# Kernel tuning notes

Measured on AMD Instinct MI355X. Metric: run time of the kernel, lower is better.

Reference implementation:

```python
import jax, jax.numpy as jnp
import numpy as np

B, A, C = 1, 196416, 90
H = W = 1024
SCORE_THRESHOLD = 0.05
MAX_DETECTIONS = 100
# RetinaNet-style BBoxTransform normalization (mean=0, std=[0.1,0.1,0.2,0.2])
STD = (0.1, 0.1, 0.2, 0.2)


def setup_inputs() -> dict:
    key = jax.random.key(0)
    k1, k2, k3, k4, k5, k6, k7 = jax.random.split(key, 7)
    x = jax.random.normal(k1, (B, 3, H, W), dtype=jnp.float32)
    regression = jax.random.normal(k2, (B, A, 4), dtype=jnp.float32) * 0.1
    classification = jax.random.normal(k3, (B, A, C), dtype=jnp.float32)
    # valid anchor boxes (x1, y1, x2, y2)
    cx = jax.random.uniform(k4, (B, A), minval=0.0, maxval=float(W))
    cy = jax.random.uniform(k5, (B, A), minval=0.0, maxval=float(H))
    aw = jax.random.uniform(k6, (B, A), minval=16.0, maxval=256.0)
    ah = jax.random.uniform(k7, (B, A), minval=16.0, maxval=256.0)
    anchors = jnp.stack([cx - 0.5 * aw, cy - 0.5 * ah, cx + 0.5 * aw, cy + 0.5 * ah], axis=2).astype(jnp.float32)
    return {"x": x, "regression": regression, "classification": classification, "anchors": anchors}


def _decode_clip(anchors, regression, img_h, img_w):
    # BBoxTransform: deltas (dx, dy, dw, dh) scaled by std, applied to anchor center/size
    wa = anchors[..., 2] - anchors[..., 0]
    ha = anchors[..., 3] - anchors[..., 1]
    cxa = anchors[..., 0] + 0.5 * wa
    cya = anchors[..., 1] + 0.5 * ha
    dx = regression[..., 0] * STD[0]
    dy = regression[..., 1] * STD[1]
    dw = regression[..., 2] * STD[2]
    dh = regression[..., 3] * STD[3]
    cx = cxa + dx * wa
    cy = cya + dy * ha
    w = jnp.exp(dw) * wa
    h = jnp.exp(dh) * ha
    # ClipBoxes: x1,y1 clamped at 0; x2,y2 clamped at image width/height
    x1 = jnp.maximum(cx - 0.5 * w, 0.0)
    y1 = jnp.maximum(cy - 0.5 * h, 0.0)
    x2 = jnp.minimum(cx + 0.5 * w, float(img_w))
    y2 = jnp.minimum(cy + 0.5 * h, float(img_h))
    return jnp.stack([x1, y1, x2, y2], axis=2)  # [B, A, 4]


def reference(x, regression, classification, anchors):
    img_h, img_w = x.shape[2], x.shape[3]
    boxes = _decode_clip(anchors, regression, img_h, img_w)  # [1, A, 4]
    probs = jax.nn.sigmoid(classification)                    # [1, A, C]
    scores = jnp.max(probs, axis=2)                           # [1, A]
    classes = jnp.argmax(probs, axis=2)                       # [1, A]
    valid_scores = jnp.where(scores > SCORE_THRESHOLD, scores, 0.0)
    vb = boxes[0]            # [A, 4]
    vc = classes[0]          # [A]
    vs = valid_scores[0]     # [A]
    k = min(MAX_DETECTIONS, vs.shape[0])
    _, top_idx = jax.lax.top_k(vs, k)
    final_boxes = vb[top_idx]
    final_scores = vs[top_idx]
    final_classes = vc[top_idx]
    return (final_boxes, final_scores, final_classes)
```

## Files before the change

kernel.cpp:

```cpp
#include <hip/hip_runtime.h>
#include <cmath>

#define A_CNT 196416
#define C_CNT 90
#define PAIRS (A_CNT / 2)
#define WITERS 12276
#define TOPK 100u
#define CAPB 2048

#define OFF_HIST1 785664u
#define OFF_CTRL  789760u
#define OFF_CANDA 789824u
#define OFF_CANDB 790336u

__global__ __launch_bounds__(256, 4) void k_reduce(const float* __restrict__ cls,
                                                   unsigned* __restrict__ keys,
                                                   unsigned* __restrict__ hist1) {
    __shared__ unsigned lhist[576];
    const int t = threadIdx.x;
    for (int j = t; j < 576; j += 256) lhist[j] = 0u;
    __syncthreads();

    const int lane = t & 63;
    const int g = lane >> 3, s = lane & 7;
    const int wid = blockIdx.x * 4 + (t >> 6);
    const int nw = gridDim.x * 4;
    const float4* __restrict__ cls4 = (const float4*)cls;

    for (int w = wid; w < WITERS; w += nw) {
        const int p = w * 8 + g;
        const float4* __restrict__ r4 = cls4 + (size_t)p * 45;
        float m0 = -INFINITY, m1 = -INFINITY;
#pragma unroll
        for (int i = 0; i < 6; ++i) {
            const int j = s + 8 * i;
            if (j < 45) {
                float4 v = r4[j];
                float a01 = fmaxf(v.x, v.y), a23 = fmaxf(v.z, v.w);
                float all = fmaxf(a01, a23);
                if (j < 22)      m0 = fmaxf(m0, all);
                else if (j > 22) m1 = fmaxf(m1, all);
                else { m0 = fmaxf(m0, a01); m1 = fmaxf(m1, a23); }
            }
        }
#pragma unroll
        for (int d = 1; d < 8; d <<= 1) {
            m0 = fmaxf(m0, __shfl_xor(m0, d));
            m1 = fmaxf(m1, __shfl_xor(m1, d));
        }
        if (s == 0) {
            float p0 = 1.0f / (1.0f + expf(-m0));
            float p1 = 1.0f / (1.0f + expf(-m1));
            unsigned k0 = (p0 > 0.05f) ? __float_as_uint(p0) : 0u;
            unsigned k1 = (p1 > 0.05f) ? __float_as_uint(p1) : 0u;
            *(uint2*)(keys + 2 * p) = make_uint2(k0, k1);
            unsigned h0 = k0 ? (min(k0 >> 16, 0x3F80u) - 0x3D4Bu) : 0u;
            unsigned h1 = k1 ? (min(k1 >> 16, 0x3F80u) - 0x3D4Bu) : 0u;
            atomicAdd(&lhist[h0], 1u);
            atomicAdd(&lhist[h1], 1u);
        }
    }
    __syncthreads();
    for (int j = t; j < 576; j += 256) {
        unsigned c = lhist[j];
        if (c) atomicAdd(&hist1[j], c);
    }
}

__global__ __launch_bounds__(256) void k_scan(const unsigned* __restrict__ hist,
                                              unsigned* __restrict__ ctrl) {
    __shared__ unsigned sdata[256];
    __shared__ unsigned sbin[2];
    const int t = threadIdx.x;
    const unsigned target = TOPK;

    uint4 u = ((const uint4*)hist)[t];
    unsigned s = u.x + u.y + u.z + u.w;
    sdata[t] = s;
    for (int d = 1; d < 256; d <<= 1) {
        __syncthreads();
        unsigned add = (t + d < 256) ? sdata[t + d] : 0u;
        __syncthreads();
        sdata[t] += add;
    }
    __syncthreads();
    {
        unsigned mysuf  = sdata[t];
        unsigned nxtsuf = (t < 255) ? sdata[t + 1] : 0u;
        if (nxtsuf < target && mysuf >= target) { sbin[0] = (unsigned)t; sbin[1] = nxtsuf; }
    }
    __syncthreads();
    const unsigned chunkB = sbin[0];
    const unsigned gAbove = sbin[1];

    unsigned v = (t < 4) ? hist[chunkB * 4 + t] : 0u;
    sdata[t] = v;
    for (int d = 1; d < 256; d <<= 1) {
        __syncthreads();
        unsigned add = (t + d < 256) ? sdata[t + d] : 0u;
        __syncthreads();
        sdata[t] += add;
    }
    __syncthreads();
    {
        unsigned mysuf  = sdata[t] + gAbove;
        unsigned nxtsuf = ((t < 255) ? sdata[t + 1] : 0u) + gAbove;
        if (nxtsuf < target && mysuf >= target) {
            unsigned bin = chunkB * 4 + (unsigned)t;
            ctrl[0] = bin ? (bin + 0x3D4Bu) : 0u;
            ctrl[1] = nxtsuf;
        }
    }
}

__global__ __launch_bounds__(256) void k_gather(const unsigned* __restrict__ keys,
                                                unsigned* __restrict__ ctrl,
                                                unsigned* __restrict__ candA,
                                                unsigned* __restrict__ candB) {
    const unsigned binB = ctrl[0];
    const int i4 = blockIdx.x * 256 + threadIdx.x;
    if (i4 >= A_CNT / 4) return;
    uint4 k = ((const uint4*)keys)[i4];
    const unsigned base = (unsigned)(4 * i4);
#pragma unroll
    for (int j = 0; j < 4; ++j) {
        unsigned kk = (j == 0) ? k.x : (j == 1) ? k.y : (j == 2) ? k.z : k.w;
        unsigned t16 = kk >> 16;
        if (t16 > binB) {
            unsigned q = atomicAdd(&ctrl[5], 1u);
            if (q < 128u) candA[q] = base + j;
        } else if (t16 == binB) {
            unsigned q = atomicAdd(&ctrl[6], 1u);
            if (q < (unsigned)CAPB) candB[q] = base + j;
        }
    }
}

__global__ __launch_bounds__(256) void k_final(const float* __restrict__ cls,
                                               const float* __restrict__ reg,
                                               const float* __restrict__ anc,
                                               const unsigned* __restrict__ ctrl,
                                               const unsigned* __restrict__ candA,
                                               const unsigned* __restrict__ candB,
                                               const unsigned* __restrict__ keys,
                                               float* __restrict__ out) {
    __shared__ unsigned sAi[128], sAk[128];
    __shared__ unsigned sBi[CAPB], sBk[CAPB];
    __shared__ unsigned sel[TOPK];
    const int t = threadIdx.x;
    const unsigned nA = min(ctrl[5], 128u);
    const unsigned nB = min(ctrl[6], (unsigned)CAPB);
    const unsigned need = TOPK - nA;

    if (t < (int)nA) { unsigned i = candA[t]; sAi[t] = i; sAk[t] = keys[i]; }
    for (unsigned e = (unsigned)t; e < nB; e += 256u) {
        unsigned i = candB[e]; sBi[e] = i; sBk[e] = keys[i];
    }
    __syncthreads();

    if (t < (int)nA) {
        unsigned mi = sAi[t], mk = sAk[t], r = 0;
        for (unsigned j = 0; j < nA; ++j) {
            unsigned ok = sAk[j];
            if (ok > mk || (ok == mk && sAi[j] < mi)) r++;
        }
        sel[r] = mi;
    }
    for (unsigned e = (unsigned)t; e < nB; e += 256u) {
        unsigned mi = sBi[e], mk = sBk[e], r = 0;
        for (unsigned j = 0; j < nB; ++j) {
            unsigned ok = sBk[j];
            if (ok > mk || (ok == mk && sBi[j] < mi)) r++;
        }
        if (r < need) sel[nA + r] = mi;
    }
    __syncthreads();

    if (t < (int)TOPK) {
        const unsigned a = sel[t];
        const float2* row = (const float2*)(cls + (size_t)a * C_CNT);
        float bv = -INFINITY; int bi = 0;
#pragma unroll 5
        for (int c = 0; c < 45; ++c) {
            float2 v = row[c];
            if (v.x > bv) { bv = v.x; bi = 2 * c; }
            if (v.y > bv) { bv = v.y; bi = 2 * c + 1; }
        }
        float score = __uint_as_float(keys[a]);
        float x1a = anc[a * 4 + 0], y1a = anc[a * 4 + 1];
        float x2a = anc[a * 4 + 2], y2a = anc[a * 4 + 3];
        float wa = x2a - x1a, ha = y2a - y1a;
        float cxa = x1a + 0.5f * wa, cya = y1a + 0.5f * ha;
        float dx = reg[a * 4 + 0] * 0.1f, dy = reg[a * 4 + 1] * 0.1f;
        float dw = reg[a * 4 + 2] * 0.2f, dh = reg[a * 4 + 3] * 0.2f;
        float cx = cxa + dx * wa, cy = cya + dy * ha;
        float w = expf(dw) * wa, h = expf(dh) * ha;
        out[t * 4 + 0] = fmaxf(cx - 0.5f * w, 0.0f);
        out[t * 4 + 1] = fmaxf(cy - 0.5f * h, 0.0f);
        out[t * 4 + 2] = fminf(cx + 0.5f * w, 1024.0f);
        out[t * 4 + 3] = fminf(cy + 0.5f * h, 1024.0f);
        out[400 + t] = score;
        out[500 + t] = (float)bi;
    }
}

extern "C" void kernel_launch(void* const* d_in, const int* in_sizes, int n_in,
                              void* d_out, int out_size, void* d_ws, size_t ws_size,
                              hipStream_t stream) {
    const float* reg = (const float*)d_in[1];
    const float* cls = (const float*)d_in[2];
    const float* anc = (const float*)d_in[3];
    float* out = (float*)d_out;
    char* ws = (char*)d_ws;
    unsigned* keys  = (unsigned*)ws;
    unsigned* hist1 = (unsigned*)(ws + OFF_HIST1);
    unsigned* ctrl  = (unsigned*)(ws + OFF_CTRL);
    unsigned* candA = (unsigned*)(ws + OFF_CANDA);
    unsigned* candB = (unsigned*)(ws + OFF_CANDB);

    hipMemsetAsync(hist1, 0, 4096 + 64, stream);
    k_reduce<<<2048, 256, 0, stream>>>(cls, keys, hist1);
    k_scan<<<1, 256, 0, stream>>>(hist1, ctrl);
    k_gather<<<192, 256, 0, stream>>>(keys, ctrl, candA, candB);
    k_final<<<1, 256, 0, stream>>>(cls, reg, anc, ctrl, candA, candB, keys, out);
}
```

Before: 160.3 us.

## Stage classification tiles in LDS with coalesced loads before row-max reduction

```diff
diff --git a/kernel.cpp b/kernel.cpp
--- a/kernel.cpp
+++ b/kernel.cpp
@@ -3,62 +3,50 @@
 
 #define A_CNT 196416
 #define C_CNT 90
-#define PAIRS (A_CNT / 2)
-#define WITERS 12276
 #define TOPK 100u
 #define CAPB 2048
+#define TB 64
+#define NTILE (A_CNT / TB)
 
 #define OFF_HIST1 785664u
 #define OFF_CTRL  789760u
 #define OFF_CANDA 789824u
 #define OFF_CANDB 790336u
 
-__global__ __launch_bounds__(256, 4) void k_reduce(const float* __restrict__ cls,
-                                                   unsigned* __restrict__ keys,
-                                                   unsigned* __restrict__ hist1) {
+__global__ __launch_bounds__(256) void k_reduce(const float* __restrict__ cls,
+                                                unsigned* __restrict__ keys,
+                                                unsigned* __restrict__ hist1) {
+    __shared__ alignas(16) float smem[TB * C_CNT];
     __shared__ unsigned lhist[576];
     const int t = threadIdx.x;
     for (int j = t; j < 576; j += 256) lhist[j] = 0u;
-    __syncthreads();
-
-    const int lane = t & 63;
-    const int g = lane >> 3, s = lane & 7;
-    const int wid = blockIdx.x * 4 + (t >> 6);
-    const int nw = gridDim.x * 4;
-    const float4* __restrict__ cls4 = (const float4*)cls;
-
-    for (int w = wid; w < WITERS; w += nw) {
-        const int p = w * 8 + g;
-        const float4* __restrict__ r4 = cls4 + (size_t)p * 45;
-        float m0 = -INFINITY, m1 = -INFINITY;
+
+    const float4* __restrict__ g4 = (const float4*)cls + (size_t)blockIdx.x * 1440;
+    float4* __restrict__ s4 = (float4*)smem;
 #pragma unroll
-        for (int i = 0; i < 6; ++i) {
-            const int j = s + 8 * i;
-            if (j < 45) {
-                float4 v = r4[j];
-                float a01 = fmaxf(v.x, v.y), a23 = fmaxf(v.z, v.w);
-                float all = fmaxf(a01, a23);
-                if (j < 22)      m0 = fmaxf(m0, all);
-                else if (j > 22) m1 = fmaxf(m1, all);
-                else { m0 = fmaxf(m0, a01); m1 = fmaxf(m1, a23); }
-            }
-        }
-#pragma unroll
-        for (int d = 1; d < 8; d <<= 1) {
-            m0 = fmaxf(m0, __shfl_xor(m0, d));
-            m1 = fmaxf(m1, __shfl_xor(m1, d));
-        }
-        if (s == 0) {
-            float p0 = 1.0f / (1.0f + expf(-m0));
-            float p1 = 1.0f / (1.0f + expf(-m1));
-            unsigned k0 = (p0 > 0.05f) ? __float_as_uint(p0) : 0u;
-            unsigned k1 = (p1 > 0.05f) ? __float_as_uint(p1) : 0u;
-            *(uint2*)(keys + 2 * p) = make_uint2(k0, k1);
-            unsigned h0 = k0 ? (min(k0 >> 16, 0x3F80u) - 0x3D4Bu) : 0u;
-            unsigned h1 = k1 ? (min(k1 >> 16, 0x3F80u) - 0x3D4Bu) : 0u;
-            atomicAdd(&lhist[h0], 1u);
-            atomicAdd(&lhist[h1], 1u);
-        }
+    for (int i = 0; i < 6; ++i) {
+        int c = t + 256 * i;
+        if (c < 1440) s4[c] = g4[c];
+    }
+    __syncthreads();
+
+    const int r = t >> 2, h = t & 3;
+    const float2* row = (const float2*)(smem + r * C_CNT) + h * 12;
+    const int n2 = (h < 3) ? 12 : 9;
+    float m = -INFINITY;
+#pragma unroll 3
+    for (int i = 0; i < n2; ++i) {
+        float2 v = row[i];
+        m = fmaxf(m, fmaxf(v.x, v.y));
+    }
+    m = fmaxf(m, __shfl_xor(m, 1));
+    m = fmaxf(m, __shfl_xor(m, 2));
+    if (h == 0) {
+        float pr = 1.0f / (1.0f + expf(-m));
+        unsigned k = (pr > 0.05f) ? __float_as_uint(pr) : 0u;
+        keys[blockIdx.x * TB + r] = k;
+        unsigned hi = k ? (min(k >> 16, 0x3F80u) - 0x3D4Bu) : 0u;
+        atomicAdd(&lhist[hi], 1u);
     }
     __syncthreads();
     for (int j = t; j < 576; j += 256) {
@@ -219,7 +207,7 @@
     unsigned* candB = (unsigned*)(ws + OFF_CANDB);
 
     hipMemsetAsync(hist1, 0, 4096 + 64, stream);
-    k_reduce<<<2048, 256, 0, stream>>>(cls, keys, hist1);
+    k_reduce<<<NTILE, 256, 0, stream>>>(cls, keys, hist1);
     k_scan<<<1, 256, 0, stream>>>(hist1, ctrl);
     k_gather<<<192, 256, 0, stream>>>(keys, ctrl, candA, candB);
     k_final<<<1, 256, 0, stream>>>(cls, reg, anc, ctrl, candA, candB, keys, out);
```

After: 168.2 us. +4.9%, slower.

## Fuse scan and final stages into preceding kernels via last-block-done counters

Applied to the files above, without the earlier changes.

```diff
diff --git a/kernel.cpp b/kernel.cpp
--- a/kernel.cpp
+++ b/kernel.cpp
@@ -7,16 +7,25 @@
 #define WITERS 12276
 #define TOPK 100u
 #define CAPB 2048
+#define NB_RED 1536
+#define NB_GAT 192
 
 #define OFF_HIST1 785664u
 #define OFF_CTRL  789760u
 #define OFF_CANDA 789824u
 #define OFF_CANDB 790336u
 
+#define AGENT_LD(p)    __hip_atomic_load((p), __ATOMIC_RELAXED, __HIP_MEMORY_SCOPE_AGENT)
+#define AGENT_ST(p, v) __hip_atomic_store((p), (v), __ATOMIC_RELAXED, __HIP_MEMORY_SCOPE_AGENT)
+
 __global__ __launch_bounds__(256, 4) void k_reduce(const float* __restrict__ cls,
                                                    unsigned* __restrict__ keys,
-                                                   unsigned* __restrict__ hist1) {
+                                                   unsigned* __restrict__ hist1,
+                                                   unsigned* __restrict__ ctrl) {
     __shared__ unsigned lhist[576];
+    __shared__ unsigned sdata[256];
+    __shared__ unsigned sbin[2];
+    __shared__ int sflag;
     const int t = threadIdx.x;
     for (int j = t; j < 576; j += 256) lhist[j] = 0u;
     __syncthreads();
@@ -24,7 +33,7 @@
     const int lane = t & 63;
     const int g = lane >> 3, s = lane & 7;
     const int wid = blockIdx.x * 4 + (t >> 6);
-    const int nw = gridDim.x * 4;
+    const int nw = NB_RED * 4;
     const float4* __restrict__ cls4 = (const float4*)cls;
 
     for (int w = wid; w < WITERS; w += nw) {
@@ -65,18 +74,16 @@
         unsigned c = lhist[j];
         if (c) atomicAdd(&hist1[j], c);
     }
-}
-
-__global__ __launch_bounds__(256) void k_scan(const unsigned* __restrict__ hist,
-                                              unsigned* __restrict__ ctrl) {
-    __shared__ unsigned sdata[256];
-    __shared__ unsigned sbin[2];
-    const int t = threadIdx.x;
+    __syncthreads();
+    if (t == 0) sflag = (atomicAdd(&ctrl[8], 1u) == NB_RED - 1u) ? 1 : 0;
+    __syncthreads();
+    if (!sflag) return;
+
     const unsigned target = TOPK;
-
-    uint4 u = ((const uint4*)hist)[t];
-    unsigned s = u.x + u.y + u.z + u.w;
-    sdata[t] = s;
+    unsigned ssum = 0;
+#pragma unroll
+    for (int j = 0; j < 4; ++j) ssum += AGENT_LD(&hist1[t * 4 + j]);
+    sdata[t] = ssum;
     for (int d = 1; d < 256; d <<= 1) {
         __syncthreads();
         unsigned add = (t + d < 256) ? sdata[t + d] : 0u;
@@ -92,8 +99,7 @@
     __syncthreads();
     const unsigned chunkB = sbin[0];
     const unsigned gAbove = sbin[1];
-
-    unsigned v = (t < 4) ? hist[chunkB * 4 + t] : 0u;
+    unsigned v = (t < 4) ? AGENT_LD(&hist1[chunkB * 4 + t]) : 0u;
     sdata[t] = v;
     for (int d = 1; d < 256; d <<= 1) {
         __syncthreads();
@@ -113,48 +119,50 @@
     }
 }
 
-__global__ __launch_bounds__(256) void k_gather(const unsigned* __restrict__ keys,
+__global__ __launch_bounds__(256) void k_gather(const float* __restrict__ cls,
+                                                const float* __restrict__ reg,
+                                                const float* __restrict__ anc,
+                                                const unsigned* __restrict__ keys,
                                                 unsigned* __restrict__ ctrl,
                                                 unsigned* __restrict__ candA,
-                                                unsigned* __restrict__ candB) {
-    const unsigned binB = ctrl[0];
-    const int i4 = blockIdx.x * 256 + threadIdx.x;
-    if (i4 >= A_CNT / 4) return;
-    uint4 k = ((const uint4*)keys)[i4];
-    const unsigned base = (unsigned)(4 * i4);
-#pragma unroll
-    for (int j = 0; j < 4; ++j) {
-        unsigned kk = (j == 0) ? k.x : (j == 1) ? k.y : (j == 2) ? k.z : k.w;
-        unsigned t16 = kk >> 16;
-        if (t16 > binB) {
-            unsigned q = atomicAdd(&ctrl[5], 1u);
-            if (q < 128u) candA[q] = base + j;
-        } else if (t16 == binB) {
-            unsigned q = atomicAdd(&ctrl[6], 1u);
-            if (q < (unsigned)CAPB) candB[q] = base + j;
-        }
-    }
-}
-
-__global__ __launch_bounds__(256) void k_final(const float* __restrict__ cls,
-                                               const float* __restrict__ reg,
-                                               const float* __restrict__ anc,
-                                               const unsigned* __restrict__ ctrl,
-                                               const unsigned* __restrict__ candA,
-                                               const unsigned* __restrict__ candB,
-                                               const unsigned* __restrict__ keys,
-                                               float* __restrict__ out) {
+                                                unsigned* __restrict__ candB,
+                                                float* __restrict__ out) {
     __shared__ unsigned sAi[128], sAk[128];
     __shared__ unsigned sBi[CAPB], sBk[CAPB];
     __shared__ unsigned sel[TOPK];
+    __shared__ int sflag;
     const int t = threadIdx.x;
-    const unsigned nA = min(ctrl[5], 128u);
-    const unsigned nB = min(ctrl[6], (unsigned)CAPB);
+
+    const unsigned binB = ctrl[0];
+    const int i4 = blockIdx.x * 256 + t;
+    if (i4 < A_CNT / 4) {
+        uint4 k = ((const uint4*)keys)[i4];
+        const unsigned base = (unsigned)(4 * i4);
+#pragma unroll
+        for (int j = 0; j < 4; ++j) {
+            unsigned kk = (j == 0) ? k.x : (j == 1) ? k.y : (j == 2) ? k.z : k.w;
+            unsigned t16 = kk >> 16;
+            if (t16 > binB) {
+                unsigned q = atomicAdd(&ctrl[5], 1u);
+                if (q < 128u) AGENT_ST(&candA[q], base + j);
+            } else if (t16 == binB) {
+                unsigned q = atomicAdd(&ctrl[6], 1u);
+                if (q < (unsigned)CAPB) AGENT_ST(&candB[q], base + j);
+            }
+        }
+    }
+    __syncthreads();
+    if (t == 0) sflag = (atomicAdd(&ctrl[9], 1u) == (unsigned)NB_GAT - 1u) ? 1 : 0;
+    __syncthreads();
+    if (!sflag) return;
+
+    const unsigned nA = min(AGENT_LD(&ctrl[5]), 128u);
+    const unsigned nB = min(AGENT_LD(&ctrl[6]), (unsigned)CAPB);
     const unsigned need = TOPK - nA;
 
-    if (t < (int)nA) { unsigned i = candA[t]; sAi[t] = i; sAk[t] = keys[i]; }
+    if (t < (int)nA) { unsigned i = AGENT_LD(&candA[t]); sAi[t] = i; sAk[t] = keys[i]; }
     for (unsigned e = (unsigned)t; e < nB; e += 256u) {
-        unsigned i = candB[e]; sBi[e] = i; sBk[e] = keys[i];
+        unsigned i = AGENT_LD(&candB[e]); sBi[e] = i; sBk[e] = keys[i];
     }
     __syncthreads();
 
@@ -219,8 +227,6 @@
     unsigned* candB = (unsigned*)(ws + OFF_CANDB);
 
     hipMemsetAsync(hist1, 0, 4096 + 64, stream);
-    k_reduce<<<2048, 256, 0, stream>>>(cls, keys, hist1);
-    k_scan<<<1, 256, 0, stream>>>(hist1, ctrl);
-    k_gather<<<192, 256, 0, stream>>>(keys, ctrl, candA, candB);
-    k_final<<<1, 256, 0, stream>>>(cls, reg, anc, ctrl, candA, candB, keys, out);
+    k_reduce<<<NB_RED, 256, 0, stream>>>(cls, keys, hist1, ctrl);
+    k_gather<<<NB_GAT, 256, 0, stream>>>(cls, reg, anc, keys, ctrl, candA, candB, out);
 }
```

New measurement: 153.1 us, median of 2. -4.5%, faster.
